# Optimization experiments

Measured on AMD Instinct MI355X. Metric: run time of the kernel, lower is better.

The kernel has to match this reference:

```python
import jax, jax.numpy as jnp
import numpy as np


def _tanh_approx(x):
    return x * jax.lax.rsqrt(1.0 + x * x)


def _lru(u, nu_log, gamma_log, Bm, Cm, Dv):
    # u: [B,T,H]; nu_log/gamma_log: [N]; Bm: [N,H]; Cm: [H,N]; Dv: [H]
    A = jnp.exp(-jnp.exp(nu_log))                       # [N], |A|<1
    Bu = jnp.exp(gamma_log) * jnp.einsum('bth,nh->btn', u, Bm)  # [B,T,N]
    A_full = jnp.broadcast_to(A, Bu.shape)
    # diagonal linear recurrence h_t = A*h_{t-1} + Bu_t via parallel scan
    def comb(c1, c2):
        a1, b1 = c1
        a2, b2 = c2
        return (a1 * a2, a2 * b1 + b2)
    _, h = jax.lax.associative_scan(comb, (A_full, Bu), axis=1)  # inclusive scan
    # module uses the state delayed by one step (out[0]=0, out[t]=h_{t-1})
    h_prev = jnp.pad(h[:, :-1, :], ((0, 0), (1, 0), (0, 0)))
    y = jnp.einsum('btn,hn->bth', h_prev, Cm) + Dv * u
    return y


def _model_block(x, nu_log, gamma_log, Bm, Cm, Dv, Wlin, blin):
    y = _lru(x, nu_log, gamma_log, Bm, Cm, Dv)
    y = _tanh_approx(y) @ Wlin.T + blin
    return y + x


def setup_inputs() -> dict:
    key = jax.random.key(0)
    ks = jax.random.split(key, 10)
    B_, T_, N, H, D = 16, 65536, 64, 64, 4
    r_min, r_max = 0.8, 1.0
    u = jax.random.uniform(ks[0], (D, N))
    nu_log = jnp.log(-0.5 * jnp.log(u * (r_max ** 2 - r_min ** 2) + r_min ** 2))
    A = jnp.exp(-jnp.exp(nu_log))
    gamma_log = jnp.log(jnp.sqrt(1.0 - A ** 2))
    Bm = jax.random.normal(ks[1], (D, N, H)) / np.sqrt(2.0 * H)
    Cm = jax.random.normal(ks[2], (D, H, N)) / np.sqrt(N)
    Dv = jax.random.normal(ks[3], (D, H))
    Wlin = jax.random.normal(ks[4], (D, H, H)) / np.sqrt(H)
    blin = jnp.zeros((D, H))
    Win = jax.random.normal(ks[5], (H, 1))
    Wout = jax.random.normal(ks[6], (1, H)) / np.sqrt(H)
    x = jax.random.normal(ks[7], (B_, T_, 1))
    return {"x": x, "Win": Win, "nu_log": nu_log, "gamma_log": gamma_log,
            "Bm": Bm, "Cm": Cm, "Dv": Dv, "Wlin": Wlin, "blin": blin, "Wout": Wout}


def reference(x, Win, nu_log, gamma_log, Bm, Cm, Dv, Wlin, blin, Wout):
    h = x @ Win.T  # [B,T,H]
    depth = nu_log.shape[0]
    for i in range(depth):
        h = _model_block(h, nu_log[i], gamma_log[i], Bm[i], Cm[i], Dv[i], Wlin[i], blin[i])
    return h @ Wout.T  # [B,T,1]
```

## Files before the change

### kernel.cpp

```cpp
#include <hip/hip_runtime.h>

#define B_ 16
#define T_ 65536
#define H_ 64
#define DEPTH_ 4
#define CHUNK 128
#define CHW 32
#define NCHW (T_ / CHW)
#define NCHB (T_ / CHUNK)

typedef _Float16 f16;
typedef f16 f16x8 __attribute__((ext_vector_type(8)));
typedef __fp16 fp16x2 __attribute__((ext_vector_type(2)));
typedef float f32x4 __attribute__((ext_vector_type(4)));
typedef unsigned u32x4 __attribute__((ext_vector_type(4)));

#define MFMA(a, b, c) __builtin_amdgcn_mfma_f32_16x16x32_f16(a, b, c, 0, 0, 0)
#define SWZ(t, k) ((t) * 64 + ((k) ^ (((t) & 7) << 2)))

union U4F8 { u32x4 u; f16x8 h; };

__device__ __forceinline__ f16x8 ldfrag(const f16* p) { return *(const f16x8*)p; }

__device__ __forceinline__ void split8(const float* vv, f16x8* hi, f16x8* lo)
{
    union { f16x8 v; fp16x2 p[4]; } H, L;
    #pragma unroll
    for (int i = 0; i < 4; ++i) {
        fp16x2 h = __builtin_amdgcn_cvt_pkrtz(vv[2 * i], vv[2 * i + 1]);
        H.p[i] = h;
        L.p[i] = __builtin_amdgcn_cvt_pkrtz(vv[2 * i] - (float)h[0],
                                            vv[2 * i + 1] - (float)h[1]);
    }
    *hi = H.v; *lo = L.v;
}

__device__ __forceinline__ f16x8 pack8(const float* vv)
{
    union { f16x8 v; fp16x2 p[4]; } H;
    #pragma unroll
    for (int i = 0; i < 4; ++i)
        H.p[i] = __builtin_amdgcn_cvt_pkrtz(vv[2 * i], vv[2 * i + 1]);
    return H.v;
}

__global__ __launch_bounds__(256)
void prep(const float* __restrict__ Win, const float* __restrict__ nu,
          const float* __restrict__ ga, const float* __restrict__ Bm,
          const float* __restrict__ Cm, const float* __restrict__ Dv,
          const float* __restrict__ Wl,
          f16* __restrict__ BmH, f16* __restrict__ BmL,
          f16* __restrict__ CmH, f16* __restrict__ CmL,
          f16* __restrict__ WlH, float* __restrict__ atab, float* __restrict__ sc)
{
    const int tid = threadIdx.x;
    for (int l = 0; l < DEPTH_; ++l) {
        for (int idx = tid; idx < 4096; idx += 256) {
            int n = idx >> 6;
            float g = expf(ga[l * 64 + n]);
            float v = Bm[l * 4096 + idx] * g;
            f16 h = (f16)v;
            BmH[l * 4096 + idx] = h;
            BmL[l * 4096 + idx] = (f16)(v - (float)h);
            float cv = Cm[l * 4096 + idx];
            h = (f16)cv;
            CmH[l * 4096 + idx] = h;
            CmL[l * 4096 + idx] = (f16)(cv - (float)h);
            WlH[l * 4096 + idx] = (f16)Wl[l * 4096 + idx];
        }
        if (tid < 64) {
            int n = tid;
            float ex = expf(nu[l * 64 + n]);
            float a = expf(-ex);
            float g = expf(ga[l * 64 + n]);
            sc[l * 320 + n] = a;
            sc[l * 320 + 64 + n] = Dv[l * 64 + n];
            float bw = 0.f;
            for (int h2 = 0; h2 < 64; ++h2) bw += Bm[l * 4096 + n * 64 + h2] * Win[h2];
            sc[l * 320 + 128 + n] = bw * g;
            sc[l * 320 + 192 + n] = Dv[l * 64 + n] * Win[n];
            sc[l * 320 + 256 + n] = Win[n];
        }
        for (int idx = tid; idx < 2048; idx += 256) {
            int n = idx >> 5, j = idx & 31;
            float ex = expf(nu[l * 64 + n]);
            atab[l * 2048 + idx] = expf(-ex * (float)j);
        }
    }
}

__global__ __launch_bounds__(64)
void carry_x(const float* __restrict__ x, const float* __restrict__ sc0,
             float* __restrict__ carry)
{
    const int blk = blockIdx.x;
    const int b = blk >> 11, c = blk & (NCHW - 1);
    const int n = threadIdx.x;
    const float a  = sc0[n];
    const float bw = sc0[128 + n];
    __shared__ float xs[CHW];
    const float* xp = x + (size_t)b * T_ + c * CHW;
    if (n < CHW) xs[n] = xp[n];
    __syncthreads();
    float s = 0.f;
    #pragma unroll
    for (int tt = 0; tt < CHW; ++tt) s = a * s + bw * xs[tt];
    carry[((size_t)b * NCHW + c) * 64 + n] = s;
}

__global__ __launch_bounds__(512)
void scan_carry(const float* __restrict__ nu_log, float* __restrict__ carry)
{
    const int b = blockIdx.x;
    const int tid = threadIdx.x;
    const int n = tid & 63, q = tid >> 6;
    const float ex = expf(nu_log[n]);
    const float aL = expf(-ex * (float)CHW);
    float* cp = carry + (size_t)b * NCHW * 64 + n;
    __shared__ float part[8][64];

    const int SEG = NCHW / 8;
    const int base = q * SEG;
    float p = 0.f;
    #pragma unroll 4
    for (int i = 0; i < SEG; ++i) {
        float v = cp[(size_t)(base + i) * 64];
        cp[(size_t)(base + i) * 64] = p;
        p = aL * p + v;
    }
    part[q][n] = p;
    __syncthreads();
    if (q > 0) {
        const float aLS = expf(-ex * (float)(CHW * SEG));
        float inc = 0.f;
        for (int qq = 0; qq < q; ++qq) inc = inc * aLS + part[qq][n];
        float qv = inc;
        #pragma unroll 4
        for (int i = 0; i < SEG; ++i) {
            cp[(size_t)(base + i) * 64] += qv;
            qv *= aL;
        }
    }
}

struct LPrep {
    const f16 *BmH, *BmL, *CmH, *CmL, *WlH;
    const float *av, *dvv, *bw, *dwin, *win;
    const f16 *BmHn, *BmLn;
    const float *atabn;
    const float *blin, *Wout;
};

template<int IN_X, int OUT_FINAL>
__global__ __launch_bounds__(256, 4)
void lru_fused(const float* __restrict__ x, f16* __restrict__ ubuf,
               LPrep P, float* __restrict__ carry, float* __restrict__ out)
{
    const int blk = blockIdx.x;
    const int b = blk >> 9, cblk = blk & (NCHB - 1);
    const int t0 = cblk * CHUNK;
    const int tid = threadIdx.x;
    const int w = tid >> 6, lane = tid & 63;
    const int l15 = lane & 15, lq = lane >> 4;
    const int cw = cblk * 4 + w;

    __shared__ float hpk[CHUNK * 64];

    f16* ug = ubuf + ((size_t)b * T_ + t0) * 64;
    const float* xg = x + (size_t)b * T_ + t0;

    float cin[4];
    #pragma unroll
    for (int nt = 0; nt < 4; ++nt)
        cin[nt] = carry[((size_t)b * NCHW + cw) * 64 + nt * 16 + l15];

    f16x8 ahu[2][2];
    if (!IN_X) {
        #pragma unroll
        for (int tt = 0; tt < 2; ++tt) {
            const f16* p = ug + (size_t)((2 * w + tt) * 16 + l15) * 64;
            ahu[tt][0] = ldfrag(p + lq * 8);
            ahu[tt][1] = ldfrag(p + 32 + lq * 8);
        }
    }

    float av4[4];
    #pragma unroll
    for (int nt = 0; nt < 4; ++nt) av4[nt] = P.av[nt * 16 + l15];

    float xv[2][4];
    if (IN_X) {
        #pragma unroll
        for (int tt = 0; tt < 2; ++tt)
            #pragma unroll
            for (int r = 0; r < 4; ++r)
                xv[tt][r] = xg[32 * w + 16 * tt + 4 * lq + r];
    }

    f32x4 acc[4][2];
    if (IN_X) {
        #pragma unroll
        for (int nt = 0; nt < 4; ++nt) {
            float bwn = P.bw[nt * 16 + l15];
            #pragma unroll
            for (int tt = 0; tt < 2; ++tt)
                #pragma unroll
                for (int r = 0; r < 4; ++r) acc[nt][tt][r] = xv[tt][r] * bwn;
        }
    } else {
        #pragma unroll
        for (int nt = 0; nt < 4; ++nt) {
            int n = nt * 16 + l15;
            f16x8 bh0 = ldfrag(P.BmH + n * 64 + lq * 8);
            f16x8 bh1 = ldfrag(P.BmH + n * 64 + 32 + lq * 8);
            f16x8 bl0 = ldfrag(P.BmL + n * 64 + lq * 8);
            f16x8 bl1 = ldfrag(P.BmL + n * 64 + 32 + lq * 8);
            #pragma unroll
            for (int tt = 0; tt < 2; ++tt) {
                f32x4 a4v = {0.f, 0.f, 0.f, 0.f};
                a4v = MFMA(ahu[tt][0], bh0, a4v);
                a4v = MFMA(ahu[tt][0], bl0, a4v);
                a4v = MFMA(ahu[tt][1], bh1, a4v);
                a4v = MFMA(ahu[tt][1], bl1, a4v);
                acc[nt][tt] = a4v;
            }
        }
    }

    float Wb[4][2];
    #pragma unroll
    for (int nt = 0; nt < 4; ++nt) {
        float a = av4[nt], a2 = a * a, a4 = a2 * a2, a8 = a4 * a4;
        float P0incl = 0.f;
        #pragma unroll
        for (int tt = 0; tt < 2; ++tt) {
            f32x4 xs = acc[nt][tt];
            float L0 = xs[0];
            float L1 = a * L0 + xs[1];
            float L2 = a * L1 + xs[2];
            float Cv = a * L2 + xs[3];
            float u1 = __shfl_up(Cv, 16);
            float t1 = Cv + ((lq >= 1) ? a4 * u1 : 0.f);
            float u2 = __shfl_up(t1, 32);
            float Pv = t1 + ((lq >= 2) ? a8 * u2 : 0.f);
            float E = __shfl_up(Pv, 16);
            E = (lq == 0) ? 0.f : E;
            if (tt == 0) { Wb[nt][0] = E; P0incl = Pv; }
            else {
                float B0 = __shfl(P0incl, 48 + l15);
                float a4lq = 1.f;
                if (lq & 1) a4lq *= a4;
                if (lq & 2) a4lq *= a8;
                Wb[nt][1] = E + a4lq * B0;
            }
        }
    }

    #pragma unroll
    for (int nt = 0; nt < 4; ++nt) {
        int n = nt * 16 + l15;
        float a = av4[nt], a2 = a * a, a4 = a2 * a2, a8 = a4 * a4, a16 = a8 * a8;
        float inc = cin[nt];
        float a4lq = 1.f;
        if (lq & 1) a4lq *= a4;
        if (lq & 2) a4lq *= a8;
        #pragma unroll
        for (int tt = 0; tt < 2; ++tt) {
            float Z = Wb[nt][tt] + a4lq * (tt ? a16 : 1.f) * inc;
            float s = Z;
            #pragma unroll
            for (int r = 0; r < 4; ++r) {
                int t = 32 * w + 16 * tt + 4 * lq + r;
                hpk[SWZ(t, n)] = s;
                s = a * s + acc[nt][tt][r];
            }
        }
    }

    #pragma unroll
    for (int tt = 0; tt < 2; ++tt) {
        int tb = 2 * w + tt, trow = tb * 16 + l15, sw = (trow & 7) << 2;
        const float* hw = hpk + trow * 64;
        f16x8 ah[2], al[2];
        #pragma unroll
        for (int kk = 0; kk < 2; ++kk) {
            int kb = kk * 32 + lq * 8;
            float4 v0 = *(const float4*)(hw + (kb ^ sw));
            float4 v1 = *(const float4*)(hw + ((kb + 4) ^ sw));
            float vv[8] = {v0.x, v0.y, v0.z, v0.w, v1.x, v1.y, v1.z, v1.w};
            split8(vv, &ah[kk], &al[kk]);
        }
        #pragma unroll
        for (int nt = 0; nt < 4; ++nt) {
            int n = nt * 16 + l15;
            f16x8 ch0 = ldfrag(P.CmH + n * 64 + lq * 8);
            f16x8 ch1 = ldfrag(P.CmH + n * 64 + 32 + lq * 8);
            f16x8 cl0 = ldfrag(P.CmL + n * 64 + lq * 8);
            f16x8 cl1 = ldfrag(P.CmL + n * 64 + 32 + lq * 8);
            f32x4 a4v = {0.f, 0.f, 0.f, 0.f};
            a4v = MFMA(ah[0], ch0, a4v);
            a4v = MFMA(al[0], ch0, a4v);
            a4v = MFMA(ah[0], cl0, a4v);
            a4v = MFMA(ah[1], ch1, a4v);
            a4v = MFMA(al[1], ch1, a4v);
            a4v = MFMA(ah[1], cl1, a4v);
            if (!IN_X) {
                float dv = P.dvv[n];
                f16 dh = (f16)dv, dl = (f16)(dv - (float)dh);
                f16x8 dfh, dfl;
                #pragma unroll
                for (int i2 = 0; i2 < 8; ++i2) { dfh[i2] = (f16)0.f; dfl[i2] = (f16)0.f; }
                int e = ((nt & 1) * 16 + l15) - lq * 8;
                if (e >= 0 && e < 8) { dfh[e] = dh; dfl[e] = dl; }
                a4v = MFMA(ahu[tt][nt >> 1], dfh, a4v);
                a4v = MFMA(ahu[tt][nt >> 1], dfl, a4v);
            }
            float dwin = IN_X ? P.dwin[n] : 0.f;
            #pragma unroll
            for (int r = 0; r < 4; ++r) {
                int t = tb * 16 + lq * 4 + r;
                float y = a4v[r];
                if (IN_X) y += xv[tt][r] * dwin;
                hpk[SWZ(t, n)] = y * rsqrtf(1.f + y * y);
            }
        }
    }

    f16* stg = (f16*)hpk;
    #pragma unroll
    for (int tt = 0; tt < 2; ++tt) {
        int tb = 2 * w + tt, trow = tb * 16 + l15, sw = (trow & 7) << 2;
        const float* hw = hpk + trow * 64;
        f16x8 t0f, t1f;
        #pragma unroll
        for (int kk = 0; kk < 2; ++kk) {
            int kb = kk * 32 + lq * 8;
            float4 v0 = *(const float4*)(hw + (kb ^ sw));
            float4 v1 = *(const float4*)(hw + ((kb + 4) ^ sw));
            float vv[8] = {v0.x, v0.y, v0.z, v0.w, v1.x, v1.y, v1.z, v1.w};
            if (kk == 0) t0f = pack8(vv); else t1f = pack8(vv);
        }
        float val[4] = {0.f, 0.f, 0.f, 0.f};
        #pragma unroll
        for (int nt = 0; nt < 4; ++nt) {
            int n = nt * 16 + l15;
            f16x8 w0f = ldfrag(P.WlH + n * 64 + lq * 8);
            f16x8 w1f = ldfrag(P.WlH + n * 64 + 32 + lq * 8);
            f32x4 a4v = {0.f, 0.f, 0.f, 0.f};
            a4v = MFMA(t0f, w0f, a4v);
            a4v = MFMA(t1f, w1f, a4v);
            if (!IN_X) {
                f16x8 ifr;
                #pragma unroll
                for (int i2 = 0; i2 < 8; ++i2) ifr[i2] = (f16)0.f;
                int e = ((nt & 1) * 16 + l15) - lq * 8;
                if (e >= 0 && e < 8) ifr[e] = (f16)1.f;
                a4v = MFMA(ahu[tt][nt >> 1], ifr, a4v);
            }
            float blj = P.blin[n];
            float wij = IN_X ? P.win[n] : 0.f;
            float woj = OUT_FINAL ? P.Wout[n] : 0.f;
            #pragma unroll
            for (int r = 0; r < 4; ++r) {
                int t = tb * 16 + lq * 4 + r;
                float o = a4v[r] + blj;
                if (IN_X) o += xv[tt][r] * wij;
                if (OUT_FINAL) {
                    val[r] += o * woj;
                } else {
                    int g = n >> 1;
                    int word = t * 64 + (((g & ~3) ^ ((t & 7) << 2)) | (g & 3));
                    stg[word * 2 + (n & 1)] = (f16)o;
                }
            }
        }
        if (OUT_FINAL) {
            #pragma unroll
            for (int r = 0; r < 4; ++r) {
                float p = val[r];
                p += __shfl_xor(p, 1);
                p += __shfl_xor(p, 2);
                p += __shfl_xor(p, 4);
                p += __shfl_xor(p, 8);
                if (l15 == 0) out[(size_t)b * T_ + t0 + tb * 16 + lq * 4 + r] = p;
            }
        }
    }

    if (!OUT_FINAL) {
        #pragma unroll
        for (int i = 0; i < 4; ++i) {
            int row = 32 * w + i * 8 + (lane >> 3);
            int gg = 4 * (lane & 7);
            int word = row * 64 + (gg ^ ((row & 7) << 2));
            u32x4 cv = *(const u32x4*)(hpk + word);
            *(u32x4*)(ug + (size_t)row * 64 + 8 * (lane & 7)) = cv;
        }

        float partial[4] = {0.f, 0.f, 0.f, 0.f};
        #pragma unroll
        for (int tt = 0; tt < 2; ++tt) {
            int tb = 2 * w + tt, arow = tb * 16 + l15, msk = (arow & 7) << 2;
            U4F8 av0, av1;
            av0.u = *(const u32x4*)(hpk + arow * 64 + ((4 * lq) ^ msk));
            av1.u = *(const u32x4*)(hpk + arow * 64 + ((16 + 4 * lq) ^ msk));
            #pragma unroll
            for (int nt = 0; nt < 4; ++nt) {
                int n = nt * 16 + l15;
                f16x8 bh0 = ldfrag(P.BmHn + n * 64 + lq * 8);
                f16x8 bh1 = ldfrag(P.BmHn + n * 64 + 32 + lq * 8);
                f16x8 bl0 = ldfrag(P.BmLn + n * 64 + lq * 8);
                f16x8 bl1 = ldfrag(P.BmLn + n * 64 + 32 + lq * 8);
                f32x4 a4v = {0.f, 0.f, 0.f, 0.f};
                a4v = MFMA(av0.h, bh0, a4v);
                a4v = MFMA(av0.h, bl0, a4v);
                a4v = MFMA(av1.h, bh1, a4v);
                a4v = MFMA(av1.h, bl1, a4v);
                float4 dp = *(const float4*)(P.atabn + n * 32 + 28 - tt * 16 - lq * 4);
                partial[nt] += a4v[0] * dp.w + a4v[1] * dp.z + a4v[2] * dp.y + a4v[3] * dp.x;
            }
        }
        #pragma unroll
        for (int nt = 0; nt < 4; ++nt) {
            float v = partial[nt];
            v += __shfl_xor(v, 16);
            v += __shfl_xor(v, 32);
            if (lq == 0)
                carry[((size_t)b * NCHW + cw) * 64 + nt * 16 + l15] = v;
        }
    }
}

extern "C" void kernel_launch(void* const* d_in, const int* in_sizes, int n_in,
                              void* d_out, int out_size, void* d_ws, size_t ws_size,
                              hipStream_t stream)
{
    const float* x   = (const float*)d_in[0];
    const float* Win = (const float*)d_in[1];
    const float* nu  = (const float*)d_in[2];
    const float* ga  = (const float*)d_in[3];
    const float* Bm  = (const float*)d_in[4];
    const float* Cm  = (const float*)d_in[5];
    const float* Dv  = (const float*)d_in[6];
    const float* Wl  = (const float*)d_in[7];
    const float* bl  = (const float*)d_in[8];
    const float* Wo  = (const float*)d_in[9];
    float* out = (float*)d_out;

    char* p = (char*)d_ws;
    f16* ubuf = (f16*)p;            p += (size_t)B_ * T_ * 64 * sizeof(f16);
    float* carry = (float*)p;       p += (size_t)B_ * NCHW * 64 * sizeof(float);
    f16* wBmH = (f16*)p;            p += 4 * 4096 * sizeof(f16);
    f16* wBmL = (f16*)p;            p += 4 * 4096 * sizeof(f16);
    f16* wCmH = (f16*)p;            p += 4 * 4096 * sizeof(f16);
    f16* wCmL = (f16*)p;            p += 4 * 4096 * sizeof(f16);
    f16* wWlH = (f16*)p;            p += 4 * 4096 * sizeof(f16);
    float* atab = (float*)p;        p += 4 * 2048 * sizeof(float);
    float* sc = (float*)p;          p += 4 * 320 * sizeof(float);

    dim3 gfused(B_ * NCHB), gcarry(B_ * NCHW), blk512(512), blk256(256), blk64(64), gscan(B_);

    prep<<<1, 256, 0, stream>>>(Win, nu, ga, Bm, Cm, Dv, Wl,
                                wBmH, wBmL, wCmH, wCmL, wWlH, atab, sc);
    carry_x<<<gcarry, blk64, 0, stream>>>(x, sc, carry);

    for (int l = 0; l < DEPTH_; ++l) {
        int ln = (l + 1 < DEPTH_) ? l + 1 : l;
        scan_carry<<<gscan, blk512, 0, stream>>>(nu + l * 64, carry);
        LPrep Pr;
        Pr.BmH = wBmH + l * 4096;  Pr.BmL = wBmL + l * 4096;
        Pr.CmH = wCmH + l * 4096;  Pr.CmL = wCmL + l * 4096;
        Pr.WlH = wWlH + l * 4096;
        Pr.av = sc + l * 320;       Pr.dvv = sc + l * 320 + 64;
        Pr.bw = sc + l * 320 + 128; Pr.dwin = sc + l * 320 + 192;
        Pr.win = sc + l * 320 + 256;
        Pr.BmHn = wBmH + ln * 4096; Pr.BmLn = wBmL + ln * 4096;
        Pr.atabn = atab + ln * 2048;
        Pr.blin = bl + l * 64; Pr.Wout = Wo;
        if (l == 0)
            lru_fused<1, 0><<<gfused, blk256, 0, stream>>>(x, ubuf, Pr, carry, out);
        else if (l == DEPTH_ - 1)
            lru_fused<0, 1><<<gfused, blk256, 0, stream>>>(x, ubuf, Pr, carry, out);
        else
            lru_fused<0, 0><<<gfused, blk256, 0, stream>>>(x, ubuf, Pr, carry, out);
    }
}
```

Before: 1.472 ms.

## Process several chunks per block with register prefetch of next chunk inputs

Each block of the fused LRU kernel now loops over consecutive chunks instead of handling one, and the grid shrinks to match. Inside the loop it issues the loads for the next chunk's carry, activations or x values ahead of the current chunk's compute, so global latency can overlap with the MFMA work. The cost is higher register pressure from the prefetch buffers and fewer blocks in the grid, which can lower occupancy and load balance.

```diff
diff --git a/kernel.cpp b/kernel.cpp
--- a/kernel.cpp
+++ b/kernel.cpp
@@ -8,6 +8,8 @@
 #define CHW 32
 #define NCHW (T_ / CHW)
 #define NCHB (T_ / CHUNK)
+#define ITER 8
+#define GRIDF (B_ * NCHB / ITER)
 
 typedef _Float16 f16;
 typedef f16 f16x8 __attribute__((ext_vector_type(8)));
@@ -156,278 +158,323 @@
 void lru_fused(const float* __restrict__ x, f16* __restrict__ ubuf,
                LPrep P, float* __restrict__ carry, float* __restrict__ out)
 {
-    const int blk = blockIdx.x;
-    const int b = blk >> 9, cblk = blk & (NCHB - 1);
-    const int t0 = cblk * CHUNK;
+    const int g = blockIdx.x;
     const int tid = threadIdx.x;
     const int w = tid >> 6, lane = tid & 63;
     const int l15 = lane & 15, lq = lane >> 4;
-    const int cw = cblk * 4 + w;
 
     __shared__ float hpk[CHUNK * 64];
-
-    f16* ug = ubuf + ((size_t)b * T_ + t0) * 64;
-    const float* xg = x + (size_t)b * T_ + t0;
-
-    float cin[4];
-    #pragma unroll
-    for (int nt = 0; nt < 4; ++nt)
-        cin[nt] = carry[((size_t)b * NCHW + cw) * 64 + nt * 16 + l15];
-
-    f16x8 ahu[2][2];
-    if (!IN_X) {
-        #pragma unroll
-        for (int tt = 0; tt < 2; ++tt) {
-            const f16* p = ug + (size_t)((2 * w + tt) * 16 + l15) * 64;
-            ahu[tt][0] = ldfrag(p + lq * 8);
-            ahu[tt][1] = ldfrag(p + 32 + lq * 8);
-        }
-    }
 
     float av4[4];
     #pragma unroll
     for (int nt = 0; nt < 4; ++nt) av4[nt] = P.av[nt * 16 + l15];
 
+    int f = g * ITER;
+    int b = f >> 9, cb = f & (NCHB - 1);
+
+    float cin[4];
+    f16x8 ahu[2][2];
     float xv[2][4];
-    if (IN_X) {
-        #pragma unroll
-        for (int tt = 0; tt < 2; ++tt)
-            #pragma unroll
-            for (int r = 0; r < 4; ++r)
-                xv[tt][r] = xg[32 * w + 16 * tt + 4 * lq + r];
-    }
-
-    f32x4 acc[4][2];
-    if (IN_X) {
+
+    {
+        const int cw = cb * 4 + w;
+        #pragma unroll
+        for (int nt = 0; nt < 4; ++nt)
+            cin[nt] = carry[((size_t)b * NCHW + cw) * 64 + nt * 16 + l15];
+        if (!IN_X) {
+            const f16* up = ubuf + ((size_t)b * T_ + cb * CHUNK) * 64;
+            #pragma unroll
+            for (int tt = 0; tt < 2; ++tt) {
+                const f16* p = up + (size_t)((2 * w + tt) * 16 + l15) * 64;
+                ahu[tt][0] = ldfrag(p + lq * 8);
+                ahu[tt][1] = ldfrag(p + 32 + lq * 8);
+            }
+        } else {
+            const float* xp = x + (size_t)b * T_ + cb * CHUNK;
+            #pragma unroll
+            for (int tt = 0; tt < 2; ++tt)
+                #pragma unroll
+                for (int r = 0; r < 4; ++r)
+                    xv[tt][r] = xp[32 * w + 16 * tt + 4 * lq + r];
+        }
+    }
+
+    for (int it = 0; it < ITER; ++it) {
+        const int t0 = cb * CHUNK;
+        const int cw = cb * 4 + w;
+        f16* ug = ubuf + ((size_t)b * T_ + t0) * 64;
+
+        int fn = f + 1; if (fn >= B_ * NCHB) fn = f;
+        int bn = fn >> 9, cn = fn & (NCHB - 1);
+        float cinN[4];
+        f16x8 ahuN[2][2];
+        float xvN[2][4];
+        {
+            const int cwn = cn * 4 + w;
+            #pragma unroll
+            for (int nt = 0; nt < 4; ++nt)
+                cinN[nt] = carry[((size_t)bn * NCHW + cwn) * 64 + nt * 16 + l15];
+            if (!IN_X) {
+                const f16* up = ubuf + ((size_t)bn * T_ + cn * CHUNK) * 64;
+                #pragma unroll
+                for (int tt = 0; tt < 2; ++tt) {
+                    const f16* p = up + (size_t)((2 * w + tt) * 16 + l15) * 64;
+                    ahuN[tt][0] = ldfrag(p + lq * 8);
+                    ahuN[tt][1] = ldfrag(p + 32 + lq * 8);
+                }
+            } else {
+                const float* xp = x + (size_t)bn * T_ + cn * CHUNK;
+                #pragma unroll
+                for (int tt = 0; tt < 2; ++tt)
+                    #pragma unroll
+                    for (int r = 0; r < 4; ++r)
+                        xvN[tt][r] = xp[32 * w + 16 * tt + 4 * lq + r];
+            }
+        }
+
+        f32x4 acc[4][2];
+        if (IN_X) {
+            #pragma unroll
+            for (int nt = 0; nt < 4; ++nt) {
+                float bwn = P.bw[nt * 16 + l15];
+                #pragma unroll
+                for (int tt = 0; tt < 2; ++tt)
+                    #pragma unroll
+                    for (int r = 0; r < 4; ++r) acc[nt][tt][r] = xv[tt][r] * bwn;
+            }
+        } else {
+            #pragma unroll
+            for (int nt = 0; nt < 4; ++nt) {
+                int n = nt * 16 + l15;
+                f16x8 bh0 = ldfrag(P.BmH + n * 64 + lq * 8);
+                f16x8 bh1 = ldfrag(P.BmH + n * 64 + 32 + lq * 8);
+                f16x8 bl0 = ldfrag(P.BmL + n * 64 + lq * 8);
+                f16x8 bl1 = ldfrag(P.BmL + n * 64 + 32 + lq * 8);
+                #pragma unroll
+                for (int tt = 0; tt < 2; ++tt) {
+                    f32x4 a4v = {0.f, 0.f, 0.f, 0.f};
+                    a4v = MFMA(ahu[tt][0], bh0, a4v);
+                    a4v = MFMA(ahu[tt][0], bl0, a4v);
+                    a4v = MFMA(ahu[tt][1], bh1, a4v);
+                    a4v = MFMA(ahu[tt][1], bl1, a4v);
+                    acc[nt][tt] = a4v;
+                }
+            }
+        }
+
+        float Wb[4][2];
         #pragma unroll
         for (int nt = 0; nt < 4; ++nt) {
-            float bwn = P.bw[nt * 16 + l15];
-            #pragma unroll
-            for (int tt = 0; tt < 2; ++tt)
-                #pragma unroll
-                for (int r = 0; r < 4; ++r) acc[nt][tt][r] = xv[tt][r] * bwn;
-        }
-    } else {
+            float a = av4[nt], a2 = a * a, a4 = a2 * a2, a8 = a4 * a4;
+            float P0incl = 0.f;
+            #pragma unroll
+            for (int tt = 0; tt < 2; ++tt) {
+                f32x4 xs = acc[nt][tt];
+                float L0 = xs[0];
+                float L1 = a * L0 + xs[1];
+                float L2 = a * L1 + xs[2];
+                float Cv = a * L2 + xs[3];
+                float u1 = __shfl_up(Cv, 16);
+                float t1 = Cv + ((lq >= 1) ? a4 * u1 : 0.f);
+                float u2 = __shfl_up(t1, 32);
+                float Pv = t1 + ((lq >= 2) ? a8 * u2 : 0.f);
+                float E = __shfl_up(Pv, 16);
+                E = (lq == 0) ? 0.f : E;
+                if (tt == 0) { Wb[nt][0] = E; P0incl = Pv; }
+                else {
+                    float B0 = __shfl(P0incl, 48 + l15);
+                    float a4lq = 1.f;
+                    if (lq & 1) a4lq *= a4;
+                    if (lq & 2) a4lq *= a8;
+                    Wb[nt][1] = E + a4lq * B0;
+                }
+            }
+        }
+
         #pragma unroll
         for (int nt = 0; nt < 4; ++nt) {
             int n = nt * 16 + l15;
-            f16x8 bh0 = ldfrag(P.BmH + n * 64 + lq * 8);
-            f16x8 bh1 = ldfrag(P.BmH + n * 64 + 32 + lq * 8);
-            f16x8 bl0 = ldfrag(P.BmL + n * 64 + lq * 8);
-            f16x8 bl1 = ldfrag(P.BmL + n * 64 + 32 + lq * 8);
+            float a = av4[nt], a2 = a * a, a4 = a2 * a2, a8 = a4 * a4, a16 = a8 * a8;
+            float inc = cin[nt];
+            float a4lq = 1.f;
+            if (lq & 1) a4lq *= a4;
+            if (lq & 2) a4lq *= a8;
             #pragma unroll
             for (int tt = 0; tt < 2; ++tt) {
-                f32x4 a4v = {0.f, 0.f, 0.f, 0.f};
-                a4v = MFMA(ahu[tt][0], bh0, a4v);
-                a4v = MFMA(ahu[tt][0], bl0, a4v);
-                a4v = MFMA(ahu[tt][1], bh1, a4v);
-                a4v = MFMA(ahu[tt][1], bl1, a4v);
-                acc[nt][tt] = a4v;
-            }
-        }
-    }
-
-    float Wb[4][2];
-    #pragma unroll
-    for (int nt = 0; nt < 4; ++nt) {
-        float a = av4[nt], a2 = a * a, a4 = a2 * a2, a8 = a4 * a4;
-        float P0incl = 0.f;
+                float Z = Wb[nt][tt] + a4lq * (tt ? a16 : 1.f) * inc;
+                float s = Z;
+                #pragma unroll
+                for (int r = 0; r < 4; ++r) {
+                    int t = 32 * w + 16 * tt + 4 * lq + r;
+                    hpk[SWZ(t, n)] = s;
+                    s = a * s + acc[nt][tt][r];
+                }
+            }
+        }
+
         #pragma unroll
         for (int tt = 0; tt < 2; ++tt) {
-            f32x4 xs = acc[nt][tt];
-            float L0 = xs[0];
-            float L1 = a * L0 + xs[1];
-            float L2 = a * L1 + xs[2];
-            float Cv = a * L2 + xs[3];
-            float u1 = __shfl_up(Cv, 16);
-            float t1 = Cv + ((lq >= 1) ? a4 * u1 : 0.f);
-            float u2 = __shfl_up(t1, 32);
-            float Pv = t1 + ((lq >= 2) ? a8 * u2 : 0.f);
-            float E = __shfl_up(Pv, 16);
-            E = (lq == 0) ? 0.f : E;
-            if (tt == 0) { Wb[nt][0] = E; P0incl = Pv; }
-            else {
-                float B0 = __shfl(P0incl, 48 + l15);
-                float a4lq = 1.f;
-                if (lq & 1) a4lq *= a4;
-                if (lq & 2) a4lq *= a8;
-                Wb[nt][1] = E + a4lq * B0;
-            }
-        }
-    }
-
-    #pragma unroll
-    for (int nt = 0; nt < 4; ++nt) {
-        int n = nt * 16 + l15;
-        float a = av4[nt], a2 = a * a, a4 = a2 * a2, a8 = a4 * a4, a16 = a8 * a8;
-        float inc = cin[nt];
-        float a4lq = 1.f;
-        if (lq & 1) a4lq *= a4;
-        if (lq & 2) a4lq *= a8;
-        #pragma unroll
-        for (int tt = 0; tt < 2; ++tt) {
-            float Z = Wb[nt][tt] + a4lq * (tt ? a16 : 1.f) * inc;
-            float s = Z;
-            #pragma unroll
-            for (int r = 0; r < 4; ++r) {
-                int t = 32 * w + 16 * tt + 4 * lq + r;
-                hpk[SWZ(t, n)] = s;
-                s = a * s + acc[nt][tt][r];
-            }
-        }
-    }
-
-    #pragma unroll
-    for (int tt = 0; tt < 2; ++tt) {
-        int tb = 2 * w + tt, trow = tb * 16 + l15, sw = (trow & 7) << 2;
-        const float* hw = hpk + trow * 64;
-        f16x8 ah[2], al[2];
-        #pragma unroll
-        for (int kk = 0; kk < 2; ++kk) {
-            int kb = kk * 32 + lq * 8;
-            float4 v0 = *(const float4*)(hw + (kb ^ sw));
-            float4 v1 = *(const float4*)(hw + ((kb + 4) ^ sw));
-            float vv[8] = {v0.x, v0.y, v0.z, v0.w, v1.x, v1.y, v1.z, v1.w};
-            split8(vv, &ah[kk], &al[kk]);
-        }
-        #pragma unroll
-        for (int nt = 0; nt < 4; ++nt) {
-            int n = nt * 16 + l15;
-            f16x8 ch0 = ldfrag(P.CmH + n * 64 + lq * 8);
-            f16x8 ch1 = ldfrag(P.CmH + n * 64 + 32 + lq * 8);
-            f16x8 cl0 = ldfrag(P.CmL + n * 64 + lq * 8);
-            f16x8 cl1 = ldfrag(P.CmL + n * 64 + 32 + lq * 8);
-            f32x4 a4v = {0.f, 0.f, 0.f, 0.f};
-            a4v = MFMA(ah[0], ch0, a4v);
-            a4v = MFMA(al[0], ch0, a4v);
-            a4v = MFMA(ah[0], cl0, a4v);
-            a4v = MFMA(ah[1], ch1, a4v);
-            a4v = MFMA(al[1], ch1, a4v);
-            a4v = MFMA(ah[1], cl1, a4v);
-            if (!IN_X) {
-                float dv = P.dvv[n];
-                f16 dh = (f16)dv, dl = (f16)(dv - (float)dh);
-                f16x8 dfh, dfl;
-                #pragma unroll
-                for (int i2 = 0; i2 < 8; ++i2) { dfh[i2] = (f16)0.f; dfl[i2] = (f16)0.f; }
-                int e = ((nt & 1) * 16 + l15) - lq * 8;
-                if (e >= 0 && e < 8) { dfh[e] = dh; dfl[e] = dl; }
-                a4v = MFMA(ahu[tt][nt >> 1], dfh, a4v);
-                a4v = MFMA(ahu[tt][nt >> 1], dfl, a4v);
-            }
-            float dwin = IN_X ? P.dwin[n] : 0.f;
-            #pragma unroll
-            for (int r = 0; r < 4; ++r) {
-                int t = tb * 16 + lq * 4 + r;
-                float y = a4v[r];
-                if (IN_X) y += xv[tt][r] * dwin;
-                hpk[SWZ(t, n)] = y * rsqrtf(1.f + y * y);
-            }
-        }
-    }
-
-    f16* stg = (f16*)hpk;
-    #pragma unroll
-    for (int tt = 0; tt < 2; ++tt) {
-        int tb = 2 * w + tt, trow = tb * 16 + l15, sw = (trow & 7) << 2;
-        const float* hw = hpk + trow * 64;
-        f16x8 t0f, t1f;
-        #pragma unroll
-        for (int kk = 0; kk < 2; ++kk) {
-            int kb = kk * 32 + lq * 8;
-            float4 v0 = *(const float4*)(hw + (kb ^ sw));
-            float4 v1 = *(const float4*)(hw + ((kb + 4) ^ sw));
-            float vv[8] = {v0.x, v0.y, v0.z, v0.w, v1.x, v1.y, v1.z, v1.w};
-            if (kk == 0) t0f = pack8(vv); else t1f = pack8(vv);
-        }
-        float val[4] = {0.f, 0.f, 0.f, 0.f};
-        #pragma unroll
-        for (int nt = 0; nt < 4; ++nt) {
-            int n = nt * 16 + l15;
-            f16x8 w0f = ldfrag(P.WlH + n * 64 + lq * 8);
-            f16x8 w1f = ldfrag(P.WlH + n * 64 + 32 + lq * 8);
-            f32x4 a4v = {0.f, 0.f, 0.f, 0.f};
-            a4v = MFMA(t0f, w0f, a4v);
-            a4v = MFMA(t1f, w1f, a4v);
-            if (!IN_X) {
-                f16x8 ifr;
-                #pragma unroll
-                for (int i2 = 0; i2 < 8; ++i2) ifr[i2] = (f16)0.f;
-                int e = ((nt & 1) * 16 + l15) - lq * 8;
-                if (e >= 0 && e < 8) ifr[e] = (f16)1.f;
-                a4v = MFMA(ahu[tt][nt >> 1], ifr, a4v);
-            }
-            float blj = P.blin[n];
-            float wij = IN_X ? P.win[n] : 0.f;
-            float woj = OUT_FINAL ? P.Wout[n] : 0.f;
-            #pragma unroll
-            for (int r = 0; r < 4; ++r) {
-                int t = tb * 16 + lq * 4 + r;
-                float o = a4v[r] + blj;
-                if (IN_X) o += xv[tt][r] * wij;
-                if (OUT_FINAL) {
-                    val[r] += o * woj;
-                } else {
-                    int g = n >> 1;
-                    int word = t * 64 + (((g & ~3) ^ ((t & 7) << 2)) | (g & 3));
-                    stg[word * 2 + (n & 1)] = (f16)o;
-                }
-            }
-        }
-        if (OUT_FINAL) {
-            #pragma unroll
-            for (int r = 0; r < 4; ++r) {
-                float p = val[r];
-                p += __shfl_xor(p, 1);
-                p += __shfl_xor(p, 2);
-                p += __shfl_xor(p, 4);
-                p += __shfl_xor(p, 8);
-                if (l15 == 0) out[(size_t)b * T_ + t0 + tb * 16 + lq * 4 + r] = p;
-            }
-        }
-    }
-
-    if (!OUT_FINAL) {
-        #pragma unroll
-        for (int i = 0; i < 4; ++i) {
-            int row = 32 * w + i * 8 + (lane >> 3);
-            int gg = 4 * (lane & 7);
-            int word = row * 64 + (gg ^ ((row & 7) << 2));
-            u32x4 cv = *(const u32x4*)(hpk + word);
-            *(u32x4*)(ug + (size_t)row * 64 + 8 * (lane & 7)) = cv;
-        }
-
-        float partial[4] = {0.f, 0.f, 0.f, 0.f};
-        #pragma unroll
-        for (int tt = 0; tt < 2; ++tt) {
-            int tb = 2 * w + tt, arow = tb * 16 + l15, msk = (arow & 7) << 2;
-            U4F8 av0, av1;
-            av0.u = *(const u32x4*)(hpk + arow * 64 + ((4 * lq) ^ msk));
-            av1.u = *(const u32x4*)(hpk + arow * 64 + ((16 + 4 * lq) ^ msk));
+            int tb = 2 * w + tt, trow = tb * 16 + l15, sw = (trow & 7) << 2;
+            const float* hw = hpk + trow * 64;
+            f16x8 ah[2], al[2];
+            #pragma unroll
+            for (int kk = 0; kk < 2; ++kk) {
+                int kb = kk * 32 + lq * 8;
+                float4 v0 = *(const float4*)(hw + (kb ^ sw));
+                float4 v1 = *(const float4*)(hw + ((kb + 4) ^ sw));
+                float vv[8] = {v0.x, v0.y, v0.z, v0.w, v1.x, v1.y, v1.z, v1.w};
+                split8(vv, &ah[kk], &al[kk]);
+            }
             #pragma unroll
             for (int nt = 0; nt < 4; ++nt) {
                 int n = nt * 16 + l15;
-                f16x8 bh0 = ldfrag(P.BmHn + n * 64 + lq * 8);
-                f16x8 bh1 = ldfrag(P.BmHn + n * 64 + 32 + lq * 8);
-                f16x8 bl0 = ldfrag(P.BmLn + n * 64 + lq * 8);
-                f16x8 bl1 = ldfrag(P.BmLn + n * 64 + 32 + lq * 8);
+                f16x8 ch0 = ldfrag(P.CmH + n * 64 + lq * 8);
+                f16x8 ch1 = ldfrag(P.CmH + n * 64 + 32 + lq * 8);
+                f16x8 cl0 = ldfrag(P.CmL + n * 64 + lq * 8);
+                f16x8 cl1 = ldfrag(P.CmL + n * 64 + 32 + lq * 8);
                 f32x4 a4v = {0.f, 0.f, 0.f, 0.f};
-                a4v = MFMA(av0.h, bh0, a4v);
-                a4v = MFMA(av0.h, bl0, a4v);
-                a4v = MFMA(av1.h, bh1, a4v);
-                a4v = MFMA(av1.h, bl1, a4v);
-                float4 dp = *(const float4*)(P.atabn + n * 32 + 28 - tt * 16 - lq * 4);
-                partial[nt] += a4v[0] * dp.w + a4v[1] * dp.z + a4v[2] * dp.y + a4v[3] * dp.x;
-            }
-        }
-        #pragma unroll
-        for (int nt = 0; nt < 4; ++nt) {
-            float v = partial[nt];
-            v += __shfl_xor(v, 16);
-            v += __shfl_xor(v, 32);
-            if (lq == 0)
-                carry[((size_t)b * NCHW + cw) * 64 + nt * 16 + l15] = v;
-        }
+                a4v = MFMA(ah[0], ch0, a4v);
+                a4v = MFMA(al[0], ch0, a4v);
+                a4v = MFMA(ah[0], cl0, a4v);
+                a4v = MFMA(ah[1], ch1, a4v);
+                a4v = MFMA(al[1], ch1, a4v);
+                a4v = MFMA(ah[1], cl1, a4v);
+                if (!IN_X) {
+                    float dv = P.dvv[n];
+                    f16 dh = (f16)dv, dl = (f16)(dv - (float)dh);
+                    f16x8 dfh, dfl;
+                    #pragma unroll
+                    for (int i2 = 0; i2 < 8; ++i2) { dfh[i2] = (f16)0.f; dfl[i2] = (f16)0.f; }
+                    int e = ((nt & 1) * 16 + l15) - lq * 8;
+                    if (e >= 0 && e < 8) { dfh[e] = dh; dfl[e] = dl; }
+                    a4v = MFMA(ahu[tt][nt >> 1], dfh, a4v);
+                    a4v = MFMA(ahu[tt][nt >> 1], dfl, a4v);
+                }
+                float dwin = IN_X ? P.dwin[n] : 0.f;
+                #pragma unroll
+                for (int r = 0; r < 4; ++r) {
+                    int t = tb * 16 + lq * 4 + r;
+                    float y = a4v[r];
+                    if (IN_X) y += xv[tt][r] * dwin;
+                    hpk[SWZ(t, n)] = y * rsqrtf(1.f + y * y);
+                }
+            }
+        }
+
+        f16* stg = (f16*)hpk;
+        #pragma unroll
+        for (int tt = 0; tt < 2; ++tt) {
+            int tb = 2 * w + tt, trow = tb * 16 + l15, sw = (trow & 7) << 2;
+            const float* hw = hpk + trow * 64;
+            f16x8 t0f, t1f;
+            #pragma unroll
+            for (int kk = 0; kk < 2; ++kk) {
+                int kb = kk * 32 + lq * 8;
+                float4 v0 = *(const float4*)(hw + (kb ^ sw));
+                float4 v1 = *(const float4*)(hw + ((kb + 4) ^ sw));
+                float vv[8] = {v0.x, v0.y, v0.z, v0.w, v1.x, v1.y, v1.z, v1.w};
+                if (kk == 0) t0f = pack8(vv); else t1f = pack8(vv);
+            }
+            float val[4] = {0.f, 0.f, 0.f, 0.f};
+            #pragma unroll
+            for (int nt = 0; nt < 4; ++nt) {
+                int n = nt * 16 + l15;
+                f16x8 w0f = ldfrag(P.WlH + n * 64 + lq * 8);
+                f16x8 w1f = ldfrag(P.WlH + n * 64 + 32 + lq * 8);
+                f32x4 a4v = {0.f, 0.f, 0.f, 0.f};
+                a4v = MFMA(t0f, w0f, a4v);
+                a4v = MFMA(t1f, w1f, a4v);
+                if (!IN_X) {
+                    f16x8 ifr;
+                    #pragma unroll
+                    for (int i2 = 0; i2 < 8; ++i2) ifr[i2] = (f16)0.f;
+                    int e = ((nt & 1) * 16 + l15) - lq * 8;
+                    if (e >= 0 && e < 8) ifr[e] = (f16)1.f;
+                    a4v = MFMA(ahu[tt][nt >> 1], ifr, a4v);
+                }
+                float blj = P.blin[n];
+                float wij = IN_X ? P.win[n] : 0.f;
+                float woj = OUT_FINAL ? P.Wout[n] : 0.f;
+                #pragma unroll
+                for (int r = 0; r < 4; ++r) {
+                    int t = tb * 16 + lq * 4 + r;
+                    float o = a4v[r] + blj;
+                    if (IN_X) o += xv[tt][r] * wij;
+                    if (OUT_FINAL) {
+                        val[r] += o * woj;
+                    } else {
+                        int gg2 = n >> 1;
+                        int word = t * 64 + (((gg2 & ~3) ^ ((t & 7) << 2)) | (gg2 & 3));
+                        stg[word * 2 + (n & 1)] = (f16)o;
+                    }
+                }
+            }
+            if (OUT_FINAL) {
+                #pragma unroll
+                for (int r = 0; r < 4; ++r) {
+                    float p = val[r];
+                    p += __shfl_xor(p, 1);
+                    p += __shfl_xor(p, 2);
+                    p += __shfl_xor(p, 4);
+                    p += __shfl_xor(p, 8);
+                    if (l15 == 0) out[(size_t)b * T_ + t0 + tb * 16 + lq * 4 + r] = p;
+                }
+            }
+        }
+
+        if (!OUT_FINAL) {
+            #pragma unroll
+            for (int i = 0; i < 4; ++i) {
+                int row = 32 * w + i * 8 + (lane >> 3);
+                int gg2 = 4 * (lane & 7);
+                int word = row * 64 + (gg2 ^ ((row & 7) << 2));
+                u32x4 cv = *(const u32x4*)(hpk + word);
+                *(u32x4*)(ug + (size_t)row * 64 + 8 * (lane & 7)) = cv;
+            }
+
+            float partial[4] = {0.f, 0.f, 0.f, 0.f};
+            #pragma unroll
+            for (int tt = 0; tt < 2; ++tt) {
+                int tb = 2 * w + tt, arow = tb * 16 + l15, msk = (arow & 7) << 2;
+                U4F8 av0, av1;
+                av0.u = *(const u32x4*)(hpk + arow * 64 + ((4 * lq) ^ msk));
+                av1.u = *(const u32x4*)(hpk + arow * 64 + ((16 + 4 * lq) ^ msk));
+                #pragma unroll
+                for (int nt = 0; nt < 4; ++nt) {
+                    int n = nt * 16 + l15;
+                    f16x8 bh0 = ldfrag(P.BmHn + n * 64 + lq * 8);
+                    f16x8 bh1 = ldfrag(P.BmHn + n * 64 + 32 + lq * 8);
+                    f16x8 bl0 = ldfrag(P.BmLn + n * 64 + lq * 8);
+                    f16x8 bl1 = ldfrag(P.BmLn + n * 64 + 32 + lq * 8);
+                    f32x4 a4v = {0.f, 0.f, 0.f, 0.f};
+                    a4v = MFMA(av0.h, bh0, a4v);
+                    a4v = MFMA(av0.h, bl0, a4v);
+                    a4v = MFMA(av1.h, bh1, a4v);
+                    a4v = MFMA(av1.h, bl1, a4v);
+                    float4 dp = *(const float4*)(P.atabn + n * 32 + 28 - tt * 16 - lq * 4);
+                    partial[nt] += a4v[0] * dp.w + a4v[1] * dp.z + a4v[2] * dp.y + a4v[3] * dp.x;
+                }
+            }
+            #pragma unroll
+            for (int nt = 0; nt < 4; ++nt) {
+                float v = partial[nt];
+                v += __shfl_xor(v, 16);
+                v += __shfl_xor(v, 32);
+                if (lq == 0)
+                    carry[((size_t)b * NCHW + cw) * 64 + nt * 16 + l15] = v;
+            }
+        }
+
+        #pragma unroll
+        for (int tt = 0; tt < 2; ++tt) {
+            ahu[tt][0] = ahuN[tt][0];
+            ahu[tt][1] = ahuN[tt][1];
+            #pragma unroll
+            for (int r = 0; r < 4; ++r) xv[tt][r] = xvN[tt][r];
+        }
+        #pragma unroll
+        for (int nt = 0; nt < 4; ++nt) cin[nt] = cinN[nt];
+        f = fn; b = bn; cb = cn;
     }
 }
 
@@ -458,7 +505,7 @@
     float* atab = (float*)p;        p += 4 * 2048 * sizeof(float);
     float* sc = (float*)p;          p += 4 * 320 * sizeof(float);
 
-    dim3 gfused(B_ * NCHB), gcarry(B_ * NCHW), blk512(512), blk256(256), blk64(64), gscan(B_);
+    dim3 gfused(GRIDF), gcarry(B_ * NCHW), blk512(512), blk256(256), blk64(64), gscan(B_);
 
     prep<<<1, 256, 0, stream>>>(Win, nu, ga, Bm, Cm, Dv, Wl,
                                 wBmH, wBmL, wCmH, wCmL, wWlH, atab, sc);
```

Measured after the change: 2.249 ms. 1.53x slower.
